# Kernel tuning notes

Hardware: AMD Instinct MI355X
Metric: run time of the kernel (lower is better)

The kernel has to match this reference:

```python
import jax, jax.numpy as jnp
import numpy as np

VOCAB = 32000
EMB = 256
UNITS = 1024


def setup_inputs() -> dict:
    key = jax.random.key(0)
    ks = jax.random.split(key, 6)
    B, S = 128, 256
    x = jax.random.randint(ks[0], (B, S), 0, VOCAB, dtype=jnp.int32)
    hidden = jnp.zeros((B, UNITS), jnp.float32)
    # Parameters (Keras GRU v2, reset_after=True): kernel W [EMB, 3*UNITS],
    # recurrent kernel U [UNITS, 3*UNITS], bias b [2, 3*UNITS] (input bias, recurrent bias)
    emb = jax.random.normal(ks[1], (VOCAB, EMB), jnp.float32) * 0.05
    W = jax.random.normal(ks[2], (EMB, 3 * UNITS), jnp.float32) * (1.0 / np.sqrt(EMB))
    U = jax.random.normal(ks[3], (UNITS, 3 * UNITS), jnp.float32) * (1.0 / np.sqrt(UNITS))
    b = jnp.zeros((2, 3 * UNITS), jnp.float32)
    return {"x": x, "hidden": hidden, "emb": emb, "W": W, "U": U, "b": b}


def _gru_seq(xp, hidden, U, b_rec):
    # xp: [S, B, 3H] precomputed input projections (incl. input bias)
    H = hidden.shape[-1]

    def step(h, xt):
        rec = h @ U + b_rec                       # [B, 3H]
        xz, xr, xh = xt[:, :H], xt[:, H:2 * H], xt[:, 2 * H:]
        rz, rr, rh = rec[:, :H], rec[:, H:2 * H], rec[:, 2 * H:]
        z = jax.nn.sigmoid(xz + rz)
        r = jax.nn.sigmoid(xr + rr)
        hh = jnp.tanh(xh + r * rh)                # reset_after=True
        h_new = z * h + (1.0 - z) * hh
        return h_new, h_new

    state, outs = jax.lax.scan(step, hidden, xp)
    return outs, state


def reference(x, hidden, emb, W, U, b):
    xe = emb[x]                                   # [B, S, EMB]
    # Precompute all input-side projections in one big GEMM
    xp = jnp.einsum('bse,eh->bsh', xe, W) + b[0]  # [B, S, 3H]
    xp = jnp.swapaxes(xp, 0, 1)                   # [S, B, 3H]
    outs, state = _gru_seq(xp, hidden, U, b[1])
    output = jnp.swapaxes(outs, 0, 1)             # [B, S, H]
    return output, state
```

## Files before the change

kernel.cpp:

```cpp
#include <hip/hip_runtime.h>

#define B_   128
#define S_   256
#define EMB_ 256
#define H_   1024
#define NH3  3072

#define G_      8
#define NW      32
#define MG      16
#define HS      32
#define THREADS 768

typedef _Float16 f16;
typedef _Float16 h8 __attribute__((ext_vector_type(8)));
typedef float    f4 __attribute__((ext_vector_type(4)));
typedef unsigned long long u64;

__global__ void gather_kernel(const int* __restrict__ x, const float* __restrict__ emb,
                              f16* __restrict__ xe16) {
  int m = blockIdx.x, k = threadIdx.x;
  int b = m & 127, s = m >> 7;
  int row = x[b * S_ + s];
  xe16[m * EMB_ + k] = (f16)emb[row * EMB_ + k];
}

__global__ void transpose_cvt(const float* __restrict__ in, f16* __restrict__ out,
                              int K, int N) {
  __shared__ float tile[32][33];
  int n0 = blockIdx.x * 32, k0 = blockIdx.y * 32;
  int tx = threadIdx.x & 31, ty = threadIdx.x >> 5;
#pragma unroll
  for (int i = 0; i < 4; ++i)
    tile[ty + 8 * i][tx] = in[(k0 + ty + 8 * i) * N + n0 + tx];
  __syncthreads();
#pragma unroll
  for (int i = 0; i < 4; ++i)
    out[(n0 + ty + 8 * i) * K + k0 + tx] = (f16)tile[tx][ty + 8 * i];
}

__launch_bounds__(THREADS, 3)
__global__ void gru_kernel(const f16* __restrict__ xe16, const f16* __restrict__ Ut,
                           const f16* __restrict__ Wt, const float* __restrict__ hidden,
                           const float* __restrict__ bvec, float* __restrict__ out,
                           f16* __restrict__ h16, int* __restrict__ ctr) {
  __shared__ f16   h_lds[MG * H_];
  __shared__ f16   xe_lds[2][MG * EMB_];
  __shared__ float recS[4][MG][100];
  __shared__ float recU[4][MG][36];

  const int tid = threadIdx.x;
  const int bid = blockIdx.x;
  const int g   = bid & 7;
  const int w   = bid >> 3;
  const int gb0 = g * MG;
  const int hc0 = w * HS;

  const int lane = tid & 63;
  const int wv   = tid >> 6;
  const int ksp  = wv & 3;
  const int cp   = wv >> 2;
  const int ln   = lane & 15;
  const int klo  = lane >> 4;
  const int bl   = tid >> 5;
  const int jl   = tid & 31;

  h8 uf0[8], uf1[8], wf0[2], wf1[2];
  {
    const f16* u0 = Ut + (size_t)(cp * H_ + hc0 + ln) * H_ + ksp * 256 + klo * 8;
    const f16* u1 = u0 + (size_t)16 * H_;
#pragma unroll
    for (int kt = 0; kt < 8; ++kt) { uf0[kt] = *(const h8*)(u0 + kt * 32);
                                     uf1[kt] = *(const h8*)(u1 + kt * 32); }
    const f16* w0 = Wt + (size_t)(cp * H_ + hc0 + ln) * EMB_ + ksp * 64 + klo * 8;
    const f16* w1 = w0 + 16 * EMB_;
#pragma unroll
    for (int kt = 0; kt < 2; ++kt) { wf0[kt] = *(const h8*)(w0 + kt * 32);
                                     wf1[kt] = *(const h8*)(w1 + kt * 32); }
  }
#pragma unroll
  for (int kt = 0; kt < 8; ++kt) { asm volatile("" : "+v"(uf0[kt])); asm volatile("" : "+v"(uf1[kt])); }
  asm volatile("" : "+v"(wf0[0]), "+v"(wf0[1]), "+v"(wf1[0]), "+v"(wf1[1]));

  float hprev = 0.f, bz = 0.f, brr = 0.f, bxh = 0.f, brh = 0.f;
  size_t obase = 0, hoff = 0;
  if (tid < 512) {
    int col = hc0 + jl;
    bz  = bvec[col] + bvec[NH3 + col];
    brr = bvec[H_ + col] + bvec[NH3 + H_ + col];
    bxh = bvec[2 * H_ + col];
    brh = bvec[NH3 + 2 * H_ + col];
    hprev = hidden[(size_t)(gb0 + bl) * H_ + col];
    obase = ((size_t)(gb0 + bl) * S_) * H_ + col;
    hoff  = (size_t)(gb0 + bl) * H_ + col;
  }

  for (int idx = tid; idx < MG * H_ / 4; idx += THREADS) {
    int r = idx >> 8, c4 = idx & 255;
    float4 hv = ((const float4*)(hidden + (size_t)(gb0 + r) * H_))[c4];
    unsigned lo = ((unsigned)__builtin_bit_cast(unsigned short, (f16)hv.y) << 16)
                |  (unsigned)__builtin_bit_cast(unsigned short, (f16)hv.x);
    unsigned hi = ((unsigned)__builtin_bit_cast(unsigned short, (f16)hv.w) << 16)
                |  (unsigned)__builtin_bit_cast(unsigned short, (f16)hv.z);
    uint2 pk = {lo, hi};
    *(uint2*)((char*)h_lds + r * 2048 + ((c4 * 8) ^ ((r & 7) << 4))) = pk;
  }
  for (int idx = tid; idx < MG * EMB_ / 8; idx += THREADS) {
    uint4 v = ((const uint4*)(xe16 + (size_t)gb0 * EMB_))[idx];
    int r = idx >> 5, c = idx & 31;
    *(uint4*)((char*)xe_lds[0] + r * 512 + ((c * 16) ^ ((r & 7) << 4))) = v;
  }
  __syncthreads();

  for (int t = 0; t < S_; ++t) {
    if (t > 0) {
      const u64* src = (const u64*)(h16 + (size_t)(t & 1) * (B_ * H_) + (size_t)gb0 * H_);
      u64 v0 = __hip_atomic_load(src + tid,               __ATOMIC_RELAXED, __HIP_MEMORY_SCOPE_AGENT);
      u64 v1 = __hip_atomic_load(src + tid + THREADS,     __ATOMIC_RELAXED, __HIP_MEMORY_SCOPE_AGENT);
      u64 v2 = __hip_atomic_load(src + tid + 2 * THREADS, __ATOMIC_RELAXED, __HIP_MEMORY_SCOPE_AGENT);
      u64 v3 = __hip_atomic_load(src + tid + 3 * THREADS, __ATOMIC_RELAXED, __HIP_MEMORY_SCOPE_AGENT);
      u64 v4 = __hip_atomic_load(src + tid + 4 * THREADS, __ATOMIC_RELAXED, __HIP_MEMORY_SCOPE_AGENT);
      u64 v5 = 0;
      if (tid < 256)
        v5 = __hip_atomic_load(src + 3840 + tid, __ATOMIC_RELAXED, __HIP_MEMORY_SCOPE_AGENT);
      { int idx = tid;               int r = idx >> 8, c = idx & 255;
        *(u64*)((char*)h_lds + r * 2048 + ((c * 8) ^ ((r & 7) << 4))) = v0; }
      { int idx = tid + THREADS;     int r = idx >> 8, c = idx & 255;
        *(u64*)((char*)h_lds + r * 2048 + ((c * 8) ^ ((r & 7) << 4))) = v1; }
      { int idx = tid + 2 * THREADS; int r = idx >> 8, c = idx & 255;
        *(u64*)((char*)h_lds + r * 2048 + ((c * 8) ^ ((r & 7) << 4))) = v2; }
      { int idx = tid + 3 * THREADS; int r = idx >> 8, c = idx & 255;
        *(u64*)((char*)h_lds + r * 2048 + ((c * 8) ^ ((r & 7) << 4))) = v3; }
      { int idx = tid + 4 * THREADS; int r = idx >> 8, c = idx & 255;
        *(u64*)((char*)h_lds + r * 2048 + ((c * 8) ^ ((r & 7) << 4))) = v4; }
      if (tid < 256) {
        int idx = 3840 + tid;        int r = idx >> 8, c = idx & 255;
        *(u64*)((char*)h_lds + r * 2048 + ((c * 8) ^ ((r & 7) << 4))) = v5;
      }
      __syncthreads();
    }

    f4 a0 = {0.f,0.f,0.f,0.f}, a1 = {0.f,0.f,0.f,0.f};
    f4 a2 = {0.f,0.f,0.f,0.f}, a3 = {0.f,0.f,0.f,0.f};
    const char* hb = (const char*)h_lds + ln * 2048;
    const char* xb = (const char*)xe_lds[t & 1] + ln * 512;
    const int rm = (ln & 7) << 4;
#pragma unroll
    for (int kt = 0; kt < 8; ++kt) {
      h8 a = *(const h8*)(hb + ((ksp * 512 + kt * 64 + klo * 16) ^ rm));
      a0 = __builtin_amdgcn_mfma_f32_16x16x32_f16(a, uf0[kt], a0, 0, 0, 0);
      a1 = __builtin_amdgcn_mfma_f32_16x16x32_f16(a, uf1[kt], a1, 0, 0, 0);
    }
#pragma unroll
    for (int kt = 0; kt < 2; ++kt) {
      h8 aw = *(const h8*)(xb + ((ksp * 128 + kt * 64 + klo * 16) ^ rm));
      a2 = __builtin_amdgcn_mfma_f32_16x16x32_f16(aw, wf0[kt], a2, 0, 0, 0);
      a3 = __builtin_amdgcn_mfma_f32_16x16x32_f16(aw, wf1[kt], a3, 0, 0, 0);
    }
#pragma unroll
    for (int j = 0; j < 4; ++j) {
      int r = klo * 4 + j;
      if (cp < 2) {
        recS[ksp][r][cp * 32 + ln]      = a0[j] + a2[j];
        recS[ksp][r][cp * 32 + 16 + ln] = a1[j] + a3[j];
      } else {
        recS[ksp][r][64 + ln] = a2[j];
        recS[ksp][r][80 + ln] = a3[j];
        recU[ksp][r][ln]      = a0[j];
        recU[ksp][r][16 + ln] = a1[j];
      }
    }
    __syncthreads();

    float outv = 0.f;
    if (tid < 512) {
      float az = recS[0][bl][jl] + recS[1][bl][jl] + recS[2][bl][jl] + recS[3][bl][jl] + bz;
      float ar = recS[0][bl][32+jl] + recS[1][bl][32+jl] + recS[2][bl][32+jl] + recS[3][bl][32+jl] + brr;
      float xh = recS[0][bl][64+jl] + recS[1][bl][64+jl] + recS[2][bl][64+jl] + recS[3][bl][64+jl] + bxh;
      float rhu = recU[0][bl][jl] + recU[1][bl][jl] + recU[2][bl][jl] + recU[3][bl][jl] + brh;
      float z  = 1.f / (1.f + __expf(-az));
      float r  = 1.f / (1.f + __expf(-ar));
      float hh = 1.f - 2.f / (1.f + __expf(2.f * (xh + r * rhu)));
      float hn = z * hprev + (1.f - z) * hh;
      hprev = hn; outv = hn;
      if (t < S_ - 1) {
        unsigned short hb16 = __builtin_bit_cast(unsigned short, (f16)hn);
        __hip_atomic_store((unsigned short*)(h16 + (size_t)((t + 1) & 1) * (B_ * H_)) + hoff,
                           hb16, __ATOMIC_RELAXED, __HIP_MEMORY_SCOPE_AGENT);
      }
    }
    if (t == S_ - 1) {
      if (tid < 512) {
        out[obase + (size_t)t * H_] = outv;
        out[(size_t)B_ * S_ * H_ + hoff] = outv;
      }
      break;
    }

    asm volatile("s_waitcnt vmcnt(0)" ::: "memory");
    __syncthreads();
    if (tid == 0)
      __hip_atomic_fetch_add(&ctr[g], 1, __ATOMIC_RELAXED, __HIP_MEMORY_SCOPE_AGENT);

    if (tid < 512) {
      out[obase + (size_t)t * H_] = outv;
    } else {
      const uint4* src = (const uint4*)(xe16 + ((size_t)(t + 1) * B_ + gb0) * EMB_);
      char* dst = (char*)xe_lds[(t + 1) & 1];
#pragma unroll
      for (int i = 0; i < 2; ++i) {
        int idx = (tid - 512) * 2 + i;
        uint4 v = src[idx];
        int r = idx >> 5, c = idx & 31;
        *(uint4*)(dst + r * 512 + ((c * 16) ^ ((r & 7) << 4))) = v;
      }
    }
    if (tid == 0) {
      int target = NW * (t + 1);
      while (__hip_atomic_load(&ctr[g], __ATOMIC_RELAXED, __HIP_MEMORY_SCOPE_AGENT) < target)
        __builtin_amdgcn_s_sleep(1);
    }
    __syncthreads();
  }
}

extern "C" void kernel_launch(void* const* d_in, const int* in_sizes, int n_in,
                              void* d_out, int out_size, void* d_ws, size_t ws_size,
                              hipStream_t stream) {
  const int*   x      = (const int*)  d_in[0];
  const float* hidden = (const float*)d_in[1];
  const float* emb    = (const float*)d_in[2];
  const float* W      = (const float*)d_in[3];
  const float* U      = (const float*)d_in[4];
  const float* bvec   = (const float*)d_in[5];
  float* out = (float*)d_out;

  char* ws = (char*)d_ws;
  f16* Ut    = (f16*)(ws);
  f16* Wt    = (f16*)(ws + 6291456);
  f16* xe16  = (f16*)(ws + 7864320);
  f16* h16   = (f16*)(ws + 24641536);
  int* ctr   = (int*)(ws + 25165824);

  hipMemsetAsync(ctr, 0, 64, stream);
  hipLaunchKernelGGL(transpose_cvt, dim3(NH3 / 32, H_ / 32), dim3(256), 0, stream,
                     U, Ut, H_, NH3);
  hipLaunchKernelGGL(transpose_cvt, dim3(NH3 / 32, EMB_ / 32), dim3(256), 0, stream,
                     W, Wt, EMB_, NH3);
  hipLaunchKernelGGL(gather_kernel, dim3(B_ * S_), dim3(EMB_), 0, stream, x, emb, xe16);

  void* args[] = { (void*)&xe16, (void*)&Ut, (void*)&Wt, (void*)&hidden,
                   (void*)&bvec, (void*)&out, (void*)&h16, (void*)&ctr };
  hipLaunchCooperativeKernel(reinterpret_cast<void*>(gru_kernel),
                             dim3(G_ * NW), dim3(THREADS), args, 0, stream);
}
```

Baseline: 1.053 ms.

## Replace counter barrier with per-element step-tagged hidden-state flags

Drops the per-group atomic counter barrier and double-buffered f16 hidden state. Each hidden value is now stored as a 32-bit word carrying its timestep tag in a triple-buffered array. Consumers spin on each word until the tag matches the expected step before writing it to LDS. This removes the vmcnt drain, an extra block barrier and the tid-0 polling, and lets data movement overlap with synchronisation, at the cost of twice the bytes per hidden element, a larger memset and per-element spinning.

```diff
diff --git a/kernel.cpp b/kernel.cpp
--- a/kernel.cpp
+++ b/kernel.cpp
@@ -15,7 +15,7 @@
 typedef _Float16 f16;
 typedef _Float16 h8 __attribute__((ext_vector_type(8)));
 typedef float    f4 __attribute__((ext_vector_type(4)));
-typedef unsigned long long u64;
+typedef unsigned int u32;
 
 __global__ void gather_kernel(const int* __restrict__ x, const float* __restrict__ emb,
                               f16* __restrict__ xe16) {
@@ -43,7 +43,7 @@
 __global__ void gru_kernel(const f16* __restrict__ xe16, const f16* __restrict__ Ut,
                            const f16* __restrict__ Wt, const float* __restrict__ hidden,
                            const float* __restrict__ bvec, float* __restrict__ out,
-                           f16* __restrict__ h16, int* __restrict__ ctr) {
+                           u32* __restrict__ htag) {
   __shared__ f16   h_lds[MG * H_];
   __shared__ f16   xe_lds[2][MG * EMB_];
   __shared__ float recS[4][MG][100];
@@ -83,7 +83,7 @@
   asm volatile("" : "+v"(wf0[0]), "+v"(wf0[1]), "+v"(wf1[0]), "+v"(wf1[1]));
 
   float hprev = 0.f, bz = 0.f, brr = 0.f, bxh = 0.f, brh = 0.f;
-  size_t obase = 0, hoff = 0;
+  size_t obase = 0, soff = 0;
   if (tid < 512) {
     int col = hc0 + jl;
     bz  = bvec[col] + bvec[NH3 + col];
@@ -92,7 +92,7 @@
     brh = bvec[NH3 + 2 * H_ + col];
     hprev = hidden[(size_t)(gb0 + bl) * H_ + col];
     obase = ((size_t)(gb0 + bl) * S_) * H_ + col;
-    hoff  = (size_t)(gb0 + bl) * H_ + col;
+    soff  = (size_t)(gb0 + bl) * H_ + col;
   }
 
   for (int idx = tid; idx < MG * H_ / 4; idx += THREADS) {
@@ -113,33 +113,6 @@
   __syncthreads();
 
   for (int t = 0; t < S_; ++t) {
-    if (t > 0) {
-      const u64* src = (const u64*)(h16 + (size_t)(t & 1) * (B_ * H_) + (size_t)gb0 * H_);
-      u64 v0 = __hip_atomic_load(src + tid,               __ATOMIC_RELAXED, __HIP_MEMORY_SCOPE_AGENT);
-      u64 v1 = __hip_atomic_load(src + tid + THREADS,     __ATOMIC_RELAXED, __HIP_MEMORY_SCOPE_AGENT);
-      u64 v2 = __hip_atomic_load(src + tid + 2 * THREADS, __ATOMIC_RELAXED, __HIP_MEMORY_SCOPE_AGENT);
-      u64 v3 = __hip_atomic_load(src + tid + 3 * THREADS, __ATOMIC_RELAXED, __HIP_MEMORY_SCOPE_AGENT);
-      u64 v4 = __hip_atomic_load(src + tid + 4 * THREADS, __ATOMIC_RELAXED, __HIP_MEMORY_SCOPE_AGENT);
-      u64 v5 = 0;
-      if (tid < 256)
-        v5 = __hip_atomic_load(src + 3840 + tid, __ATOMIC_RELAXED, __HIP_MEMORY_SCOPE_AGENT);
-      { int idx = tid;               int r = idx >> 8, c = idx & 255;
-        *(u64*)((char*)h_lds + r * 2048 + ((c * 8) ^ ((r & 7) << 4))) = v0; }
-      { int idx = tid + THREADS;     int r = idx >> 8, c = idx & 255;
-        *(u64*)((char*)h_lds + r * 2048 + ((c * 8) ^ ((r & 7) << 4))) = v1; }
-      { int idx = tid + 2 * THREADS; int r = idx >> 8, c = idx & 255;
-        *(u64*)((char*)h_lds + r * 2048 + ((c * 8) ^ ((r & 7) << 4))) = v2; }
-      { int idx = tid + 3 * THREADS; int r = idx >> 8, c = idx & 255;
-        *(u64*)((char*)h_lds + r * 2048 + ((c * 8) ^ ((r & 7) << 4))) = v3; }
-      { int idx = tid + 4 * THREADS; int r = idx >> 8, c = idx & 255;
-        *(u64*)((char*)h_lds + r * 2048 + ((c * 8) ^ ((r & 7) << 4))) = v4; }
-      if (tid < 256) {
-        int idx = 3840 + tid;        int r = idx >> 8, c = idx & 255;
-        *(u64*)((char*)h_lds + r * 2048 + ((c * 8) ^ ((r & 7) << 4))) = v5;
-      }
-      __syncthreads();
-    }
-
     f4 a0 = {0.f,0.f,0.f,0.f}, a1 = {0.f,0.f,0.f,0.f};
     f4 a2 = {0.f,0.f,0.f,0.f}, a3 = {0.f,0.f,0.f,0.f};
     const char* hb = (const char*)h_lds + ln * 2048;
@@ -184,27 +157,19 @@
       float hn = z * hprev + (1.f - z) * hh;
       hprev = hn; outv = hn;
       if (t < S_ - 1) {
-        unsigned short hb16 = __builtin_bit_cast(unsigned short, (f16)hn);
-        __hip_atomic_store((unsigned short*)(h16 + (size_t)((t + 1) & 1) * (B_ * H_)) + hoff,
-                           hb16, __ATOMIC_RELAXED, __HIP_MEMORY_SCOPE_AGENT);
-      }
+        u32 word = ((u32)(t + 1) << 16)
+                 | (u32)__builtin_bit_cast(unsigned short, (f16)hn);
+        __hip_atomic_store(htag + (size_t)((t + 1) % 3) * (B_ * H_) + soff, word,
+                           __ATOMIC_RELAXED, __HIP_MEMORY_SCOPE_AGENT);
+      }
+      out[obase + (size_t)t * H_] = outv;
     }
     if (t == S_ - 1) {
-      if (tid < 512) {
-        out[obase + (size_t)t * H_] = outv;
-        out[(size_t)B_ * S_ * H_ + hoff] = outv;
-      }
+      if (tid < 512) out[(size_t)B_ * S_ * H_ + soff] = outv;
       break;
     }
 
-    asm volatile("s_waitcnt vmcnt(0)" ::: "memory");
-    __syncthreads();
-    if (tid == 0)
-      __hip_atomic_fetch_add(&ctr[g], 1, __ATOMIC_RELAXED, __HIP_MEMORY_SCOPE_AGENT);
-
-    if (tid < 512) {
-      out[obase + (size_t)t * H_] = outv;
-    } else {
+    if (tid >= 512) {
       const uint4* src = (const uint4*)(xe16 + ((size_t)(t + 1) * B_ + gb0) * EMB_);
       char* dst = (char*)xe_lds[(t + 1) & 1];
 #pragma unroll
@@ -214,11 +179,24 @@
         int r = idx >> 5, c = idx & 31;
         *(uint4*)(dst + r * 512 + ((c * 16) ^ ((r & 7) << 4))) = v;
       }
-    }
-    if (tid == 0) {
-      int target = NW * (t + 1);
-      while (__hip_atomic_load(&ctr[g], __ATOMIC_RELAXED, __HIP_MEMORY_SCOPE_AGENT) < target)
-        __builtin_amdgcn_s_sleep(1);
+    } else {
+      const u32* src = htag + ((size_t)((t + 1) % 3) * B_ + gb0) * H_ + (tid << 1);
+      const u32 tg = (u32)(t + 1);
+      u32 va[16], vb[16];
+#pragma unroll
+      for (int r = 0; r < 16; ++r) {
+        va[r] = __hip_atomic_load(src + r * H_,     __ATOMIC_RELAXED, __HIP_MEMORY_SCOPE_AGENT);
+        vb[r] = __hip_atomic_load(src + r * H_ + 1, __ATOMIC_RELAXED, __HIP_MEMORY_SCOPE_AGENT);
+      }
+#pragma unroll
+      for (int r = 0; r < 16; ++r) {
+        while ((va[r] >> 16) != tg)
+          va[r] = __hip_atomic_load(src + r * H_,     __ATOMIC_RELAXED, __HIP_MEMORY_SCOPE_AGENT);
+        while ((vb[r] >> 16) != tg)
+          vb[r] = __hip_atomic_load(src + r * H_ + 1, __ATOMIC_RELAXED, __HIP_MEMORY_SCOPE_AGENT);
+        u32 pk = (va[r] & 0xffffu) | (vb[r] << 16);
+        *(u32*)((char*)h_lds + r * 2048 + ((tid * 4) ^ ((r & 7) << 4))) = pk;
+      }
     }
     __syncthreads();
   }
@@ -239,10 +217,9 @@
   f16* Ut    = (f16*)(ws);
   f16* Wt    = (f16*)(ws + 6291456);
   f16* xe16  = (f16*)(ws + 7864320);
-  f16* h16   = (f16*)(ws + 24641536);
-  int* ctr   = (int*)(ws + 25165824);
-
-  hipMemsetAsync(ctr, 0, 64, stream);
+  u32* htag  = (u32*)(ws + 24641536);
+
+  hipMemsetAsync(htag, 0, 3 * B_ * H_ * 4, stream);
   hipLaunchKernelGGL(transpose_cvt, dim3(NH3 / 32, H_ / 32), dim3(256), 0, stream,
                      U, Ut, H_, NH3);
   hipLaunchKernelGGL(transpose_cvt, dim3(NH3 / 32, EMB_ / 32), dim3(256), 0, stream,
@@ -250,7 +227,7 @@
   hipLaunchKernelGGL(gather_kernel, dim3(B_ * S_), dim3(EMB_), 0, stream, x, emb, xe16);
 
   void* args[] = { (void*)&xe16, (void*)&Ut, (void*)&Wt, (void*)&hidden,
-                   (void*)&bvec, (void*)&out, (void*)&h16, (void*)&ctr };
+                   (void*)&bvec, (void*)&out, (void*)&htag };
   hipLaunchCooperativeKernel(reinterpret_cast<void*>(gru_kernel),
                              dim3(G_ * NW), dim3(THREADS), args, 0, stream);
 }
```

New measurement: 3.249 ms. 209% more time.
